# Optimization experiments

Measured on AMD Instinct MI355X. Metric: run time of the kernel, lower is better.

The kernel has to match this reference:

```python
import jax, jax.numpy as jnp
import numpy as np

N = 8000      # nodes
E = 64000     # edges
F = 2560      # in_channels
H = 8         # heads
C = 320       # out_channels per head
G = 16        # graphs in batch
SLOPE = 0.2   # GATv2 default negative_slope


def setup_inputs() -> dict:
    key = jax.random.key(0)
    ks = jax.random.split(key, 20)
    inp = {
        'x': jax.random.normal(ks[0], (N, F), jnp.float32),
        'edge_index': jax.random.randint(ks[1], (2, E), 0, N, dtype=jnp.int64),
        'edge_attr': jax.random.normal(ks[2], (E, 1), jnp.float32),
        'batch': jnp.sort(jax.random.randint(ks[3], (N,), 0, G, dtype=jnp.int64)),
    }
    s_in = 1.0 / np.sqrt(F).astype(np.float32)
    s_att = 1.0 / np.sqrt(C).astype(np.float32)
    k = 4
    for layer in (1, 2):
        inp[f'Wl{layer}'] = jax.random.normal(ks[k + 0], (F, H * C), jnp.float32) * s_in
        inp[f'bl{layer}'] = jnp.zeros((H * C,), jnp.float32)
        inp[f'Wr{layer}'] = jax.random.normal(ks[k + 1], (F, H * C), jnp.float32) * s_in
        inp[f'br{layer}'] = jnp.zeros((H * C,), jnp.float32)
        inp[f'We{layer}'] = jax.random.normal(ks[k + 2], (1, H * C), jnp.float32)
        inp[f'att{layer}'] = jax.random.normal(ks[k + 3], (H, C), jnp.float32) * s_att
        inp[f'bias{layer}'] = jnp.zeros((H * C,), jnp.float32)
        k += 4
    return inp


def gatv2_layer(x, src, dst, edge_attr, Wl, bl, Wr, br, We, att, bias):
    # x: [N,F] -> out: [N, H*C]
    xl = (x @ Wl + bl).reshape(N, H, C)   # source transform (aggregated)
    xr = (x @ Wr + br).reshape(N, H, C)   # target transform
    ee = (edge_attr @ We).reshape(E, H, C)
    m = jax.nn.leaky_relu(xl[src] + xr[dst] + ee, SLOPE)  # [E,H,C]
    score = jnp.einsum('ehc,hc->eh', m, att)               # [E,H]
    # segment softmax over incoming edges of each target node
    smax = jax.ops.segment_max(score, dst, num_segments=N)  # [N,H]
    ex = jnp.exp(score - smax[dst])
    denom = jax.ops.segment_sum(ex, dst, num_segments=N)    # [N,H]
    alpha = ex / denom[dst]                                  # [E,H]
    out = jax.ops.segment_sum(xl[src] * alpha[:, :, None], dst, num_segments=N)
    return out.reshape(N, H * C) + bias


def reference(x, edge_index, edge_attr, batch,
              Wl1, bl1, Wr1, br1, We1, att1, bias1,
              Wl2, bl2, Wr2, br2, We2, att2, bias2):
    src, dst = edge_index[0], edge_index[1]
    h = gatv2_layer(x, src, dst, edge_attr, Wl1, bl1, Wr1, br1, We1, att1, bias1)
    # dropout is identity in eval mode
    h = gatv2_layer(h, src, dst, edge_attr, Wl2, bl2, Wr2, br2, We2, att2, bias2)
    # global mean pool over graphs
    sums = jax.ops.segment_sum(h, batch, num_segments=G)                 # [G, H*C]
    cnt = jax.ops.segment_sum(jnp.ones((N, 1), h.dtype), batch, num_segments=G)
    return sums / jnp.maximum(cnt, 1.0)
```

## Files before the change

### kernel.cpp

```cpp
#include <hip/hip_runtime.h>

typedef unsigned short u16;
typedef _Float16 f16;
typedef _Float16 f16x8 __attribute__((ext_vector_type(8)));
typedef float f32x4 __attribute__((ext_vector_type(4)));

#define AS1 __attribute__((address_space(1)))
#define AS3 __attribute__((address_space(3)))

constexpr int N_NODES = 8000;
constexpr int N_EDGES = 64000;
constexpr int F_IN    = 2560;
constexpr int HEADS   = 8;
constexpr int CPH     = 320;
constexpr int HC      = 2560;
constexpr int NW      = 5120;
constexpr int NGRAPH  = 16;
constexpr float SLOPE = 0.2f;

__global__ __launch_bounds__(256)
void cvt_f32_f16(const float* __restrict__ in, f16* __restrict__ out, int n)
{
  const int i = (blockIdx.x * 256 + threadIdx.x) * 4;
  if (i >= n) return;
  const float4 v = *(const float4*)(in + i);
  f16 o[4] = {(f16)v.x, (f16)v.y, (f16)v.z, (f16)v.w};
  *(ushort4*)(out + i) = *(const ushort4*)o;
}

__global__ __launch_bounds__(256)
void transpose_w(const float* __restrict__ in, f16* __restrict__ out)
{
  __shared__ u16 tile[64][66];
  const int bx = blockIdx.x * 64;
  const int by = blockIdx.y * 64;
  const int tx = threadIdx.x & 63;
  const int ty = threadIdx.x >> 6;
  #pragma unroll
  for (int i = ty; i < 64; i += 4) {
    f16 h = (f16)in[(size_t)(by + i) * HC + bx + tx];
    u16 u; __builtin_memcpy(&u, &h, 2);
    tile[i][tx] = u;
  }
  __syncthreads();
  #pragma unroll
  for (int i = ty; i < 64; i += 4) {
    u16 u = tile[tx][i];
    f16 h; __builtin_memcpy(&h, &u, 2);
    out[(size_t)(bx + i) * F_IN + by + tx] = h;
  }
}

__global__ __launch_bounds__(512)
void gemm_fused(const f16* __restrict__ A, const f16* __restrict__ BT,
                const float* __restrict__ bl, const float* __restrict__ br,
                f16* __restrict__ XL, f16* __restrict__ XR, int M)
{
  __shared__ __align__(16) f16 sA[256 * 32];
  __shared__ __align__(16) f16 sB[128 * 32];
  const int t    = threadIdx.x;
  const int lane = t & 63;
  const int wave = t >> 6;
  const int m0 = (blockIdx.x & 31) * 256;
  const int n0 = (blockIdx.x >> 5) * 128;
  const int fm = (wave >> 1) * 64;
  const int fn = (wave & 1) * 64;
  const int ml = lane & 15;
  const int lq = lane >> 4;

  f32x4 acc[4][4] = {};

  for (int k0 = 0; k0 < F_IN; k0 += 32) {
    __syncthreads();
    #pragma unroll
    for (int j = 0; j < 2; ++j) {
      const int s = j * 512 + t;
      const int r = s >> 2;
      const int lc = (s & 3) ^ ((r >> 1) & 3);
      int ra = m0 + r; ra = (ra < M) ? ra : (M - 1);
      const f16* ga = A + (size_t)ra * F_IN + k0 + lc * 8;
      __builtin_amdgcn_global_load_lds((AS1 const void*)ga,
                                       (AS3 void*)(sA + s * 8), 16, 0, 0);
    }
    {
      const int s = t;
      const int r = s >> 2;
      const int lc = (s & 3) ^ ((r >> 1) & 3);
      const f16* gb = BT + (size_t)(n0 + r) * F_IN + k0 + lc * 8;
      __builtin_amdgcn_global_load_lds((AS1 const void*)gb,
                                       (AS3 void*)(sB + s * 8), 16, 0, 0);
    }
    __syncthreads();

    f16x8 af[4], bfr[4];
    #pragma unroll
    for (int i = 0; i < 4; ++i) {
      const int row = fm + i * 16 + ml;
      const int p = lq ^ ((row >> 1) & 3);
      af[i] = *(const f16x8*)(sA + (row * 4 + p) * 8);
    }
    #pragma unroll
    for (int j = 0; j < 4; ++j) {
      const int row = fn + j * 16 + ml;
      const int p = lq ^ ((row >> 1) & 3);
      bfr[j] = *(const f16x8*)(sB + (row * 4 + p) * 8);
    }

    #pragma unroll
    for (int i = 0; i < 4; ++i)
      #pragma unroll
      for (int j = 0; j < 4; ++j)
        acc[i][j] = __builtin_amdgcn_mfma_f32_16x16x32_f16(af[i], bfr[j], acc[i][j], 0, 0, 0);
  }

  const bool left = (n0 < HC);
  f16* __restrict__ OUT = left ? XL : XR;
  const float* __restrict__ bias = left ? bl : br;
  const int nb = left ? n0 : (n0 - HC);
  const int rg = (lane >> 4) * 4;
  #pragma unroll
  for (int j = 0; j < 4; ++j) {
    const int gn = nb + fn + j * 16 + ml;
    const float bv = bias[gn];
    #pragma unroll
    for (int i = 0; i < 4; ++i) {
      #pragma unroll
      for (int r = 0; r < 4; ++r) {
        const int gm = m0 + fm + i * 16 + rg + r;
        if (gm < M) OUT[(size_t)gm * HC + gn] = (f16)(acc[i][j][r] + bv);
      }
    }
  }
}

__global__ __launch_bounds__(256)
void count_edges(const int* __restrict__ dst, int* __restrict__ counts)
{
  const int e = blockIdx.x * 256 + threadIdx.x;
  if (e < N_EDGES) atomicAdd(&counts[dst[e]], 1);
}

__global__ __launch_bounds__(256)
void scan_offsets(const int* __restrict__ counts, int* __restrict__ offs, int* __restrict__ cur)
{
  __shared__ int wtot[4];
  const int t = threadIdx.x;
  const int lane = t & 63, wave = t >> 6;
  const int base = t * 32;
  int loc[32];
  int run = 0;
  #pragma unroll
  for (int i = 0; i < 32; ++i) {
    const int idx = base + i;
    const int v = (idx < N_NODES) ? counts[idx] : 0;
    loc[i] = run;
    run += v;
  }
  int incl = run;
  #pragma unroll
  for (int off = 1; off < 64; off <<= 1) {
    int y = __shfl_up(incl, off, 64);
    if (lane >= off) incl += y;
  }
  const int excl = incl - run;
  if (lane == 63) wtot[wave] = incl;
  __syncthreads();
  int wb = 0;
  for (int wv = 0; wv < wave; ++wv) wb += wtot[wv];
  const int mybase = wb + excl;
  #pragma unroll
  for (int i = 0; i < 32; ++i) {
    const int idx = base + i;
    if (idx < N_NODES) { offs[idx] = mybase + loc[i]; cur[idx] = mybase + loc[i]; }
  }
  if (t == 255) offs[N_NODES] = wb + incl;
}

__global__ __launch_bounds__(256)
void fill_csr(const int* __restrict__ dst, int* __restrict__ cur, int* __restrict__ eids)
{
  const int e = blockIdx.x * 256 + threadIdx.x;
  if (e < N_EDGES) {
    const int p = atomicAdd(&cur[dst[e]], 1);
    eids[p] = e;
  }
}

__global__ __launch_bounds__(256)
void gat_edge_fused(const f16* __restrict__ XL, const f16* __restrict__ XR,
                    const float* __restrict__ We, const float* __restrict__ att,
                    const float* __restrict__ eattr,
                    const int* __restrict__ src,
                    const int* __restrict__ offs, const int* __restrict__ eids,
                    const float* __restrict__ bias,
                    f16* __restrict__ out)
{
  const int n    = blockIdx.x;
  const int t    = threadIdx.x;
  const int wave = t >> 6;
  const int lane = t & 63;
  const int half = lane >> 5;
  const int l32  = lane & 31;
  const int h    = wave * 2 + half;
  const int cb   = h * CPH + l32;

  float xr[10], wv[10], av[10];
  #pragma unroll
  for (int k = 0; k < 10; ++k) {
    const int c = cb + 32 * k;
    xr[k] = (float)XR[(size_t)n * HC + c];
    wv[k] = We[c];
    av[k] = att[c];
  }

  float m = -3.0e38f, l = 0.f;
  float acc[10];
  #pragma unroll
  for (int k = 0; k < 10; ++k) acc[k] = 0.f;

  const int b = offs[n], e = offs[n + 1];
  for (int p = b; p < e; ++p) {
    const int eid  = eids[p];
    const int s    = src[eid];
    const float ea = eattr[eid];
    const f16* row = XL + (size_t)s * HC;
    float xl[10];
    float partial = 0.f;
    #pragma unroll
    for (int k = 0; k < 10; ++k) {
      xl[k] = (float)row[cb + 32 * k];
      float v = xl[k] + xr[k] + ea * wv[k];
      v = (v > 0.f) ? v : SLOPE * v;
      partial += v * av[k];
    }
    #pragma unroll
    for (int msk = 16; msk >= 1; msk >>= 1)
      partial += __shfl_xor(partial, msk, 64);
    const float sc    = partial;
    const float mn    = fmaxf(m, sc);
    const float scale = __expf(m - mn);
    const float w     = __expf(sc - mn);
    l = l * scale + w;
    #pragma unroll
    for (int k = 0; k < 10; ++k) acc[k] = acc[k] * scale + w * xl[k];
    m = mn;
  }

  const float inv = (l > 0.f) ? 1.f / l : 0.f;
  #pragma unroll
  for (int k = 0; k < 10; ++k) {
    const int c = cb + 32 * k;
    out[(size_t)n * HC + c] = (f16)(acc[k] * inv + bias[c]);
  }
}

__global__ __launch_bounds__(256)
void pool_kernel(const f16* __restrict__ Hm, const int* __restrict__ batch, float* __restrict__ out)
{
  __shared__ int se[2];
  const int g = blockIdx.x;
  const int chunk = blockIdx.y;
  const int t = threadIdx.x;
  if (t < 2) {
    const int target = g + t;
    int lo = 0, hi = N_NODES;
    while (lo < hi) { const int mid = (lo + hi) >> 1; if (batch[mid] < target) lo = mid + 1; else hi = mid; }
    se[t] = lo;
  }
  __syncthreads();
  const int s0 = se[0], s1 = se[1];
  const int c = chunk * 256 + t;
  float sum = 0.f;
  for (int n = s0; n < s1; ++n) sum += (float)Hm[(size_t)n * HC + c];
  int cnt = s1 - s0; if (cnt < 1) cnt = 1;
  out[g * HC + c] = sum / (float)cnt;
}

static void run_layer(const f16* A, const float* Wl, const float* bl,
                      const float* Wr, const float* br,
                      const float* We, const float* att, const float* bias,
                      const int* src, const float* eattr,
                      f16* WT, f16* XL, f16* XR,
                      const int* offs, const int* eids, f16* OUT, hipStream_t stream)
{
  dim3 tgrid(HC / 64, F_IN / 64);
  transpose_w<<<tgrid, 256, 0, stream>>>(Wl, WT);
  transpose_w<<<tgrid, 256, 0, stream>>>(Wr, WT + (size_t)HC * F_IN);
  gemm_fused<<<32 * (NW / 128), 512, 0, stream>>>(A, WT, bl, br, XL, XR, N_NODES);
  gat_edge_fused<<<N_NODES, 256, 0, stream>>>(XL, XR, We, att, eattr, src, offs, eids, bias, OUT);
}

extern "C" void kernel_launch(void* const* d_in, const int* in_sizes, int n_in,
                              void* d_out, int out_size, void* d_ws, size_t ws_size,
                              hipStream_t stream)
{
  const float* x     = (const float*)d_in[0];
  const int*   eidx  = (const int*)d_in[1];
  const float* eattr = (const float*)d_in[2];
  const int*   batch = (const int*)d_in[3];
  const float* Wl1  = (const float*)d_in[4];
  const float* bl1  = (const float*)d_in[5];
  const float* Wr1  = (const float*)d_in[6];
  const float* br1  = (const float*)d_in[7];
  const float* We1  = (const float*)d_in[8];
  const float* att1 = (const float*)d_in[9];
  const float* bias1= (const float*)d_in[10];
  const float* Wl2  = (const float*)d_in[11];
  const float* bl2  = (const float*)d_in[12];
  const float* Wr2  = (const float*)d_in[13];
  const float* br2  = (const float*)d_in[14];
  const float* We2  = (const float*)d_in[15];
  const float* att2 = (const float*)d_in[16];
  const float* bias2= (const float*)d_in[17];
  float* out = (float*)d_out;

  const int* src = eidx;
  const int* dst = eidx + N_EDGES;

  char* w = (char*)d_ws;
  auto take = [&](size_t b) { char* p = w; w += (b + 255) & ~(size_t)255; return p; };
  f16*   Xh    = (f16*)take((size_t)N_NODES * F_IN * 2);
  f16*   H2h   = (f16*)take((size_t)N_NODES * HC * 2);
  f16*   WT    = (f16*)take((size_t)NW * F_IN * 2);
  f16*   XL    = (f16*)take((size_t)N_NODES * HC * 2);
  f16*   XR    = (f16*)take((size_t)N_NODES * HC * 2);
  int*   counts= (int*)take((size_t)N_NODES * 4);
  int*   offs  = (int*)take((size_t)(N_NODES + 1) * 4);
  int*   cur   = (int*)take((size_t)N_NODES * 4);
  int*   eids  = (int*)take((size_t)N_EDGES * 4);

  hipMemsetAsync(counts, 0, N_NODES * 4, stream);
  count_edges<<<N_EDGES / 256, 256, 0, stream>>>(dst, counts);
  scan_offsets<<<1, 256, 0, stream>>>(counts, offs, cur);
  fill_csr<<<N_EDGES / 256, 256, 0, stream>>>(dst, cur, eids);

  cvt_f32_f16<<<(N_NODES * F_IN) / 1024, 256, 0, stream>>>(x, Xh, N_NODES * F_IN);

  run_layer(Xh, Wl1, bl1, Wr1, br1, We1, att1, bias1, src, eattr,
            WT, XL, XR, offs, eids, Xh, stream);
  run_layer(Xh, Wl2, bl2, Wr2, br2, We2, att2, bias2, src, eattr,
            WT, XL, XR, offs, eids, H2h, stream);

  pool_kernel<<<dim3(NGRAPH, HC / 256), 256, 0, stream>>>(H2h, batch, out);
}
```

Before: 1.048 ms.

## Retile GEMM to 192x128 with 4 waves and vectorize edge kernel loads

The GEMM block tile changes from 256x128 with 8 waves to 192x128 with 4 waves. Each wave now holds 6x4 MFMA accumulators, so reuse per wave goes up, and the grid grows to 42 M-tiles, which changes tail and occupancy behaviour. Separately, the edge attention kernel reads and writes two adjacent f16 channels per lane (f16x2/float2) instead of scalar elements, cutting the number of memory instructions in the gather. The risks are higher register pressure in the GEMM and fewer waves per block to hide latency.

```diff
diff --git a/kernel.cpp b/kernel.cpp
--- a/kernel.cpp
+++ b/kernel.cpp
@@ -2,6 +2,7 @@
 
 typedef unsigned short u16;
 typedef _Float16 f16;
+typedef _Float16 f16x2 __attribute__((ext_vector_type(2)));
 typedef _Float16 f16x8 __attribute__((ext_vector_type(8)));
 typedef float f32x4 __attribute__((ext_vector_type(4)));
 
@@ -17,6 +18,7 @@
 constexpr int NW      = 5120;
 constexpr int NGRAPH  = 16;
 constexpr float SLOPE = 0.2f;
+constexpr int MT      = 42;
 
 __global__ __launch_bounds__(256)
 void cvt_f32_f16(const float* __restrict__ in, f16* __restrict__ out, int n)
@@ -51,30 +53,32 @@
   }
 }
 
-__global__ __launch_bounds__(512)
+__global__ __launch_bounds__(256)
 void gemm_fused(const f16* __restrict__ A, const f16* __restrict__ BT,
                 const float* __restrict__ bl, const float* __restrict__ br,
                 f16* __restrict__ XL, f16* __restrict__ XR, int M)
 {
-  __shared__ __align__(16) f16 sA[256 * 32];
+  __shared__ __align__(16) f16 sA[192 * 32];
   __shared__ __align__(16) f16 sB[128 * 32];
   const int t    = threadIdx.x;
   const int lane = t & 63;
   const int wave = t >> 6;
-  const int m0 = (blockIdx.x & 31) * 256;
-  const int n0 = (blockIdx.x >> 5) * 128;
-  const int fm = (wave >> 1) * 64;
+  const int mt = blockIdx.x % MT;
+  const int nt = blockIdx.x / MT;
+  const int m0 = mt * 192;
+  const int n0 = nt * 128;
+  const int fm = (wave >> 1) * 96;
   const int fn = (wave & 1) * 64;
   const int ml = lane & 15;
   const int lq = lane >> 4;
 
-  f32x4 acc[4][4] = {};
+  f32x4 acc[6][4] = {};
 
   for (int k0 = 0; k0 < F_IN; k0 += 32) {
     __syncthreads();
     #pragma unroll
-    for (int j = 0; j < 2; ++j) {
-      const int s = j * 512 + t;
+    for (int j = 0; j < 3; ++j) {
+      const int s = j * 256 + t;
       const int r = s >> 2;
       const int lc = (s & 3) ^ ((r >> 1) & 3);
       int ra = m0 + r; ra = (ra < M) ? ra : (M - 1);
@@ -82,8 +86,9 @@
       __builtin_amdgcn_global_load_lds((AS1 const void*)ga,
                                        (AS3 void*)(sA + s * 8), 16, 0, 0);
     }
-    {
-      const int s = t;
+    #pragma unroll
+    for (int j = 0; j < 2; ++j) {
+      const int s = j * 256 + t;
       const int r = s >> 2;
       const int lc = (s & 3) ^ ((r >> 1) & 3);
       const f16* gb = BT + (size_t)(n0 + r) * F_IN + k0 + lc * 8;
@@ -92,9 +97,9 @@
     }
     __syncthreads();
 
-    f16x8 af[4], bfr[4];
-    #pragma unroll
-    for (int i = 0; i < 4; ++i) {
+    f16x8 af[6], bfr[4];
+    #pragma unroll
+    for (int i = 0; i < 6; ++i) {
       const int row = fm + i * 16 + ml;
       const int p = lq ^ ((row >> 1) & 3);
       af[i] = *(const f16x8*)(sA + (row * 4 + p) * 8);
@@ -107,7 +112,7 @@
     }
 
     #pragma unroll
-    for (int i = 0; i < 4; ++i)
+    for (int i = 0; i < 6; ++i)
       #pragma unroll
       for (int j = 0; j < 4; ++j)
         acc[i][j] = __builtin_amdgcn_mfma_f32_16x16x32_f16(af[i], bfr[j], acc[i][j], 0, 0, 0);
@@ -123,7 +128,7 @@
     const int gn = nb + fn + j * 16 + ml;
     const float bv = bias[gn];
     #pragma unroll
-    for (int i = 0; i < 4; ++i) {
+    for (int i = 0; i < 6; ++i) {
       #pragma unroll
       for (int r = 0; r < 4; ++r) {
         const int gm = m0 + fm + i * 16 + rg + r;
@@ -202,21 +207,22 @@
   const int half = lane >> 5;
   const int l32  = lane & 31;
   const int h    = wave * 2 + half;
-  const int cb   = h * CPH + l32;
-
-  float xr[10], wv[10], av[10];
-  #pragma unroll
-  for (int k = 0; k < 10; ++k) {
-    const int c = cb + 32 * k;
-    xr[k] = (float)XR[(size_t)n * HC + c];
-    wv[k] = We[c];
-    av[k] = att[c];
+  const int cb   = h * CPH + 2 * l32;
+
+  float2 xr[5], wv[5], av[5];
+  #pragma unroll
+  for (int k = 0; k < 5; ++k) {
+    const int c = cb + 64 * k;
+    const f16x2 p = *(const f16x2*)(XR + (size_t)n * HC + c);
+    xr[k] = make_float2((float)p.x, (float)p.y);
+    wv[k] = *(const float2*)(We + c);
+    av[k] = *(const float2*)(att + c);
   }
 
   float m = -3.0e38f, l = 0.f;
-  float acc[10];
-  #pragma unroll
-  for (int k = 0; k < 10; ++k) acc[k] = 0.f;
+  float acc0[5], acc1[5];
+  #pragma unroll
+  for (int k = 0; k < 5; ++k) { acc0[k] = 0.f; acc1[k] = 0.f; }
 
   const int b = offs[n], e = offs[n + 1];
   for (int p = b; p < e; ++p) {
@@ -224,14 +230,18 @@
     const int s    = src[eid];
     const float ea = eattr[eid];
     const f16* row = XL + (size_t)s * HC;
-    float xl[10];
+    float xl0[5], xl1[5];
     float partial = 0.f;
     #pragma unroll
-    for (int k = 0; k < 10; ++k) {
-      xl[k] = (float)row[cb + 32 * k];
-      float v = xl[k] + xr[k] + ea * wv[k];
-      v = (v > 0.f) ? v : SLOPE * v;
-      partial += v * av[k];
+    for (int k = 0; k < 5; ++k) {
+      const f16x2 q = *(const f16x2*)(row + cb + 64 * k);
+      xl0[k] = (float)q.x;
+      xl1[k] = (float)q.y;
+      float v0 = xl0[k] + xr[k].x + ea * wv[k].x;
+      float v1 = xl1[k] + xr[k].y + ea * wv[k].y;
+      v0 = (v0 > 0.f) ? v0 : SLOPE * v0;
+      v1 = (v1 > 0.f) ? v1 : SLOPE * v1;
+      partial += v0 * av[k].x + v1 * av[k].y;
     }
     #pragma unroll
     for (int msk = 16; msk >= 1; msk >>= 1)
@@ -242,15 +252,21 @@
     const float w     = __expf(sc - mn);
     l = l * scale + w;
     #pragma unroll
-    for (int k = 0; k < 10; ++k) acc[k] = acc[k] * scale + w * xl[k];
+    for (int k = 0; k < 5; ++k) {
+      acc0[k] = acc0[k] * scale + w * xl0[k];
+      acc1[k] = acc1[k] * scale + w * xl1[k];
+    }
     m = mn;
   }
 
   const float inv = (l > 0.f) ? 1.f / l : 0.f;
   #pragma unroll
-  for (int k = 0; k < 10; ++k) {
-    const int c = cb + 32 * k;
-    out[(size_t)n * HC + c] = (f16)(acc[k] * inv + bias[c]);
+  for (int k = 0; k < 5; ++k) {
+    const int c = cb + 64 * k;
+    f16x2 o;
+    o.x = (f16)(acc0[k] * inv + bias[c]);
+    o.y = (f16)(acc1[k] * inv + bias[c + 1]);
+    *(f16x2*)(out + (size_t)n * HC + c) = o;
   }
 }
 
@@ -286,7 +302,7 @@
   dim3 tgrid(HC / 64, F_IN / 64);
   transpose_w<<<tgrid, 256, 0, stream>>>(Wl, WT);
   transpose_w<<<tgrid, 256, 0, stream>>>(Wr, WT + (size_t)HC * F_IN);
-  gemm_fused<<<32 * (NW / 128), 512, 0, stream>>>(A, WT, bl, br, XL, XR, N_NODES);
+  gemm_fused<<<MT * (NW / 128), 256, 0, stream>>>(A, WT, bl, br, XL, XR, N_NODES);
   gat_edge_fused<<<N_NODES, 256, 0, stream>>>(XL, XR, We, att, eattr, src, offs, eids, bias, OUT);
 }
 
```

After: 1.609 ms. 53.5% more time.
